# Kernel tuning notes

Hardware: AMD Instinct MI355X
Metric: run time of the kernel (lower is better)

The kernel has to match this reference:

```python
import jax, jax.numpy as jnp
import numpy as np

SEQ, BATCH, HID = 2048, 4, 1024


def setup_inputs() -> dict:
    key = jax.random.key(0)
    ks = jax.random.split(key, 8)
    s = 1.0 / np.sqrt(HID)
    return {
        "x": jax.random.normal(ks[0], (SEQ, BATCH, HID), dtype=jnp.float32),
        "ssm": jax.random.uniform(ks[1], (BATCH, SEQ, SEQ), dtype=jnp.float32),
        "Wq": jax.random.uniform(ks[2], (HID, HID), jnp.float32, -s, s),
        "bq": jax.random.uniform(ks[3], (HID,), jnp.float32, -s, s),
        "Wk": jax.random.uniform(ks[4], (HID, HID), jnp.float32, -s, s),
        "bk": jax.random.uniform(ks[5], (HID,), jnp.float32, -s, s),
        "Wv": jax.random.uniform(ks[6], (HID, HID), jnp.float32, -s, s),
        "bv": jax.random.uniform(ks[7], (HID,), jnp.float32, -s, s),
    }


def reference(x, ssm, Wq, bq, Wk, bk, Wv, bv):
    # x: [seq, batch, hid]; torch Linear: y = x @ W.T + b
    scale = jnp.asarray(HID ** 0.5, x.dtype)
    Q = x @ Wq.T + bq                      # [s, b, h]
    K = x @ Wk.T + bk
    V = x @ Wv.T + bv
    # transpose to batch-first: [b, s, h]
    Q = jnp.transpose(Q, (1, 0, 2))
    K = jnp.transpose(K, (1, 0, 2))
    V = jnp.transpose(V, (1, 0, 2))
    scores = jnp.einsum('bqh,bkh->bqk', Q, K) / scale   # [b, s, s]
    masked = scores * ssm                                # multiplicative mask on raw scores
    attn = jax.nn.softmax(masked, axis=-1)
    out = jnp.einsum('bqk,bkh->bqh', attn, V)            # [b, s, h]
    return jnp.transpose(out, (1, 0, 2))                 # [s, b, h]
```

## Files before the change

### kernel.cpp

```cpp
#include <hip/hip_runtime.h>
#include <hip/hip_bf16.h>

#define SEQ 2048
#define BATCH 4
#define HID 1024

typedef __bf16 bf16x8 __attribute__((ext_vector_type(8)));
typedef __bf16 bf16x4 __attribute__((ext_vector_type(4)));
typedef float f32x4 __attribute__((ext_vector_type(4)));

__device__ __forceinline__ void gload_lds16(void* lds, const void* g) {
  __builtin_amdgcn_global_load_lds(
      (const __attribute__((address_space(1))) void*)g,
      (__attribute__((address_space(3))) void*)lds, 16, 0, 0);
}

__global__ __launch_bounds__(256) void cast_f32_bf16(const float* __restrict__ in,
                                                     __bf16* __restrict__ out, int n8) {
  int i = blockIdx.x * 256 + threadIdx.x;
  if (i >= n8) return;
  const float4* p = (const float4*)in + (size_t)i * 2;
  float4 a = p[0], b = p[1];
  bf16x8 v;
  v[0] = (__bf16)a.x; v[1] = (__bf16)a.y; v[2] = (__bf16)a.z; v[3] = (__bf16)a.w;
  v[4] = (__bf16)b.x; v[5] = (__bf16)b.y; v[6] = (__bf16)b.z; v[7] = (__bf16)b.w;
  ((bf16x8*)out)[i] = v;
}

__global__ __launch_bounds__(256) void cast_w3(const float* __restrict__ w0,
                                               const float* __restrict__ w1,
                                               const float* __restrict__ w2,
                                               __bf16* __restrict__ out) {
  const int wsel = blockIdx.y;
  const float* src = wsel == 0 ? w0 : wsel == 1 ? w1 : w2;
  int i = blockIdx.x * 256 + threadIdx.x;
  const float4* p = (const float4*)src + (size_t)i * 2;
  float4 a = p[0], b = p[1];
  bf16x8 v;
  v[0] = (__bf16)a.x; v[1] = (__bf16)a.y; v[2] = (__bf16)a.z; v[3] = (__bf16)a.w;
  v[4] = (__bf16)b.x; v[5] = (__bf16)b.y; v[6] = (__bf16)b.z; v[7] = (__bf16)b.w;
  ((bf16x8*)(out + (size_t)wsel * HID * HID))[i] = v;
}

__global__ void concat_bias(const float* b0, const float* b1, const float* b2,
                            float* __restrict__ out) {
  const float* s = blockIdx.x == 0 ? b0 : blockIdx.x == 1 ? b1 : b2;
  out[blockIdx.x * HID + threadIdx.x] = s[threadIdx.x];
}

#define SLOT 49152
template<int EPI>
__global__ __launch_bounds__(512, 2)
void gemm8(const __bf16* __restrict__ A, int lda, long long sAz,
           const __bf16* __restrict__ B, int ldb, long long sBz,
           const float* __restrict__ aux, void* __restrict__ dst,
           float* __restrict__ aux2, int K)
{
  __shared__ __align__(16) char lds[3 * SLOT];
  const int tid = threadIdx.x;
  const int wid = tid >> 6, lane = tid & 63;
  const int wr = wid >> 2, wc = wid & 3;
  const int m0 = blockIdx.x * 128, n0 = blockIdx.y * 256;
  const int z = blockIdx.z;
  const __bf16* Ab = A + (size_t)z * sAz;
  const __bf16* Bb = B + (size_t)z * sBz;

  const int srow = tid >> 3;
  const int scol = ((tid & 7) * 16) ^ ((srow & 7) << 4);
  const char* asrc0 = (const char*)(Ab + (size_t)(m0 + srow) * lda) + scol;
  const char* asrc1 = (const char*)(Ab + (size_t)(m0 + srow + 64) * lda) + scol;
  const char* bsrc0 = (const char*)(Bb + (size_t)(n0 + srow) * ldb) + scol;
  const char* bsrc1 = (const char*)(Bb + (size_t)(n0 + srow + 64) * ldb) + scol;
  const char* bsrc2 = (const char*)(Bb + (size_t)(n0 + srow + 128) * ldb) + scol;
  const char* bsrc3 = (const char*)(Bb + (size_t)(n0 + srow + 192) * ldb) + scol;
  const int dA = tid * 16, dB = 16384 + tid * 16;

  const int fr = lane & 15, fq = lane >> 4;
  const int fc2 = fq * 16;
  const int swz = (fr & 7) << 4;
  int aoff[4][2], boff[4][2];
#pragma unroll
  for (int mi = 0; mi < 4; ++mi) {
    const int row = wr * 64 + mi * 16 + fr;
#pragma unroll
    for (int ks = 0; ks < 2; ++ks)
      aoff[mi][ks] = row * 128 + ((fc2 + ks * 64) ^ swz);
  }
#pragma unroll
  for (int ni = 0; ni < 4; ++ni) {
    const int row = wc * 64 + ni * 16 + fr;
#pragma unroll
    for (int ks = 0; ks < 2; ++ks)
      boff[ni][ks] = 16384 + row * 128 + ((fc2 + ks * 64) ^ swz);
  }

  const int nk = K >> 6;
  {
    char* s0 = lds;
    gload_lds16(s0 + dA, asrc0); gload_lds16(s0 + dA + 8192, asrc1);
    gload_lds16(s0 + dB, bsrc0); gload_lds16(s0 + dB + 8192, bsrc1);
    gload_lds16(s0 + dB + 16384, bsrc2); gload_lds16(s0 + dB + 24576, bsrc3);
    char* s1 = lds + SLOT;
    gload_lds16(s1 + dA, asrc0 + 128); gload_lds16(s1 + dA + 8192, asrc1 + 128);
    gload_lds16(s1 + dB, bsrc0 + 128); gload_lds16(s1 + dB + 8192, bsrc1 + 128);
    gload_lds16(s1 + dB + 16384, bsrc2 + 128); gload_lds16(s1 + dB + 24576, bsrc3 + 128);
  }

  f32x4 acc[4][4] = {};
  for (int t = 0; t < nk; ++t) {
    char* s = lds + (t % 3) * SLOT;
    if (t + 1 < nk) asm volatile("s_waitcnt vmcnt(6)" ::: "memory");
    else            asm volatile("s_waitcnt vmcnt(0)" ::: "memory");
    __builtin_amdgcn_s_barrier();
    asm volatile("" ::: "memory");

    bf16x8 a[4][2], b[4][2];
#pragma unroll
    for (int mi = 0; mi < 4; ++mi)
#pragma unroll
      for (int ks = 0; ks < 2; ++ks)
        a[mi][ks] = *(const bf16x8*)(s + aoff[mi][ks]);
#pragma unroll
    for (int ni = 0; ni < 2; ++ni)
#pragma unroll
      for (int ks = 0; ks < 2; ++ks)
        b[ni][ks] = *(const bf16x8*)(s + boff[ni][ks]);
    if (t + 2 < nk) {
      char* sn = lds + ((t + 2) % 3) * SLOT;
      const size_t ko = (size_t)(t + 2) * 128;
      gload_lds16(sn + dA, asrc0 + ko);
      gload_lds16(sn + dA + 8192, asrc1 + ko);
      gload_lds16(sn + dB, bsrc0 + ko);
    }
    asm volatile("" ::: "memory");
    __builtin_amdgcn_s_barrier();
    asm volatile("s_waitcnt lgkmcnt(0)" ::: "memory");
    __builtin_amdgcn_sched_barrier(0);
    __builtin_amdgcn_s_setprio(1);
#pragma unroll
    for (int mi = 0; mi < 4; ++mi)
#pragma unroll
      for (int ni = 0; ni < 2; ++ni)
#pragma unroll
        for (int ks = 0; ks < 2; ++ks)
          acc[mi][ni] = __builtin_amdgcn_mfma_f32_16x16x32_bf16(a[mi][ks], b[ni][ks], acc[mi][ni], 0, 0, 0);
    __builtin_amdgcn_s_setprio(0);
    asm volatile("" ::: "memory");
    __builtin_amdgcn_s_barrier();
    asm volatile("" ::: "memory");

#pragma unroll
    for (int ni = 2; ni < 4; ++ni)
#pragma unroll
      for (int ks = 0; ks < 2; ++ks)
        b[ni][ks] = *(const bf16x8*)(s + boff[ni][ks]);
    if (t + 2 < nk) {
      char* sn = lds + ((t + 2) % 3) * SLOT;
      const size_t ko = (size_t)(t + 2) * 128;
      gload_lds16(sn + dB + 8192, bsrc1 + ko);
      gload_lds16(sn + dB + 16384, bsrc2 + ko);
      gload_lds16(sn + dB + 24576, bsrc3 + ko);
    }
    asm volatile("" ::: "memory");
    __builtin_amdgcn_s_barrier();
    asm volatile("s_waitcnt lgkmcnt(0)" ::: "memory");
    __builtin_amdgcn_sched_barrier(0);
    __builtin_amdgcn_s_setprio(1);
#pragma unroll
    for (int mi = 0; mi < 4; ++mi)
#pragma unroll
      for (int ni = 2; ni < 4; ++ni)
#pragma unroll
        for (int ks = 0; ks < 2; ++ks)
          acc[mi][ni] = __builtin_amdgcn_mfma_f32_16x16x32_bf16(a[mi][ks], b[ni][ks], acc[mi][ni], 0, 0, 0);
    __builtin_amdgcn_s_setprio(0);
  }
  __syncthreads();

  if (EPI == 0) {
    const int hsel = n0 >> 10;
    const size_t BSH = (size_t)BATCH * SEQ * HID;
#pragma unroll
    for (int mi = 0; mi < 4; ++mi) {
#pragma unroll
      for (int ni = 0; ni < 4; ++ni) {
        const int gn = n0 + wc * 64 + ni * 16 + fr;
        const int h = gn & (HID - 1);
        const int gmb = m0 + wr * 64 + mi * 16 + fq * 4;
        const float bias = aux[gn];
        f32x4 v = acc[mi][ni];
        if (hsel < 2) {
#pragma unroll
          for (int r = 0; r < 4; ++r)
            ((__bf16*)dst)[(size_t)hsel * BSH + (size_t)z * SEQ * HID +
                           (size_t)(gmb + r) * HID + h] = (__bf16)(v[r] + bias);
        } else {
          bf16x4 vv;
#pragma unroll
          for (int r = 0; r < 4; ++r) vv[r] = (__bf16)(v[r] + bias);
          *(bf16x4*)&((__bf16*)dst)[2 * BSH + (size_t)z * HID * SEQ +
                                    (size_t)h * SEQ + gmb] = vv;
        }
      }
    }
  } else if (EPI == 2) {
    float psum[4][4] = {};
#pragma unroll
    for (int mi = 0; mi < 4; ++mi) {
#pragma unroll
      for (int ni = 0; ni < 4; ++ni) {
        const int gn = n0 + wc * 64 + ni * 16 + fr;
        const int gmb = m0 + wr * 64 + mi * 16 + fq * 4;
        f32x4 v = acc[mi][ni];
#pragma unroll
        for (int r = 0; r < 4; ++r) {
          const size_t idx = (size_t)z * SEQ * SEQ + (size_t)(gmb + r) * SEQ + gn;
          const float e = __expf(v[r] * 0.03125f * aux[idx]);
          ((__bf16*)dst)[idx] = (__bf16)e;
          psum[mi][r] += e;
        }
      }
    }
#pragma unroll
    for (int mi = 0; mi < 4; ++mi)
#pragma unroll
      for (int r = 0; r < 4; ++r) {
        float sv = psum[mi][r];
        sv += __shfl_xor(sv, 1); sv += __shfl_xor(sv, 2);
        sv += __shfl_xor(sv, 4); sv += __shfl_xor(sv, 8);
        psum[mi][r] = sv;
      }
    float* red = (float*)lds;
    if (fr == 0) {
#pragma unroll
      for (int mi = 0; mi < 4; ++mi)
#pragma unroll
        for (int r = 0; r < 4; ++r)
          red[wid * 64 + mi * 16 + fq * 4 + r] = psum[mi][r];
    }
    __syncthreads();
    if (tid < 128) {
      const int half = tid >> 6, r64 = tid & 63;
      float sv = 0.f;
#pragma unroll
      for (int j = 0; j < 4; ++j) sv += red[(half * 4 + j) * 64 + r64];
      aux2[((size_t)z * SEQ + m0 + tid) * 8 + blockIdx.y] = sv;
    }
  } else {
    float* red = (float*)lds;
    if (tid < 128) {
      const float* pp = aux + ((size_t)z * SEQ + m0 + tid) * 8;
      float sv = 0.f;
#pragma unroll
      for (int j = 0; j < 8; ++j) sv += pp[j];
      red[tid] = 1.f / sv;
    }
    __syncthreads();
#pragma unroll
    for (int mi = 0; mi < 4; ++mi) {
#pragma unroll
      for (int ni = 0; ni < 4; ++ni) {
        const int gn = n0 + wc * 64 + ni * 16 + fr;
        const int rbase = wr * 64 + mi * 16 + fq * 4;
        f32x4 v = acc[mi][ni];
#pragma unroll
        for (int r = 0; r < 4; ++r)
          ((float*)dst)[((size_t)(m0 + rbase + r) * BATCH + z) * HID + gn] = v[r] * red[rbase + r];
      }
    }
  }
}

extern "C" void kernel_launch(void* const* d_in, const int* in_sizes, int n_in,
                              void* d_out, int out_size, void* d_ws, size_t ws_size,
                              hipStream_t stream) {
  const float* x   = (const float*)d_in[0];
  const float* ssm = (const float*)d_in[1];
  const float* Wq  = (const float*)d_in[2];
  const float* bq  = (const float*)d_in[3];
  const float* Wk  = (const float*)d_in[4];
  const float* bk  = (const float*)d_in[5];
  const float* Wv  = (const float*)d_in[6];
  const float* bv  = (const float*)d_in[7];
  float* out = (float*)d_out;

  const size_t BSH = (size_t)BATCH * SEQ * HID;
  float* bqkv    = (float*)d_ws;
  float* partial = bqkv + 4096;
  __bf16* xbf  = (__bf16*)(partial + (size_t)BATCH * SEQ * 8);
  __bf16* wqkv = xbf + BSH;
  __bf16* Qb = wqkv + (size_t)3 * HID * HID;
  __bf16* Kb = Qb + BSH;
  __bf16* Vt = Qb + 2 * BSH;
  __bf16* E  = Qb + 3 * BSH;

  cast_f32_bf16<<<(int)(BSH / 8 / 256), 256, 0, stream>>>(x, xbf, (int)(BSH / 8));
  cast_w3<<<dim3(HID * HID / 8 / 256, 3), 256, 0, stream>>>(Wq, Wk, Wv, wqkv);
  concat_bias<<<3, HID, 0, stream>>>(bq, bk, bv, bqkv);

  gemm8<0><<<dim3(16, 12, BATCH), 512, 0, stream>>>(xbf, BATCH * HID, HID,
                                                    wqkv, HID, 0, bqkv, Qb, nullptr, HID);
  gemm8<2><<<dim3(16, 8, BATCH), 512, 0, stream>>>(Qb, HID, (long long)SEQ * HID,
                                                   Kb, HID, (long long)SEQ * HID,
                                                   ssm, E, partial, HID);
  gemm8<3><<<dim3(16, 4, BATCH), 512, 0, stream>>>(E, SEQ, (long long)SEQ * SEQ,
                                                   Vt, SEQ, (long long)HID * SEQ,
                                                   partial, out, nullptr, SEQ);
}
```

Baseline: 165.4 us.

## Enlarge GEMM tiles to 256 rows with double-buffered four-phase MFMA schedule

Replaces the 128x256 triple-buffered GEMM with a templated 256xNW*64 tile kernel that uses two LDS buffers and splits each K-step into four MFMA phases interleaved with staged loads. The QKV projection now treats x as a flat 8192-row matrix instead of batching over z, and the epilogue remaps rows to batch/seq. The PV GEMM uses a narrower 256x128 tile. The aim is more data reuse per LDS load and fewer blocks, at the cost of more accumulator registers (risking spills at 2 blocks/CU), double rather than triple buffering, and scalar V-transposed stores in the QKV epilogue.

```diff
diff --git a/kernel.cpp b/kernel.cpp
--- a/kernel.cpp
+++ b/kernel.cpp
@@ -6,7 +6,6 @@
 #define HID 1024
 
 typedef __bf16 bf16x8 __attribute__((ext_vector_type(8)));
-typedef __bf16 bf16x4 __attribute__((ext_vector_type(4)));
 typedef float f32x4 __attribute__((ext_vector_type(4)));
 
 __device__ __forceinline__ void gload_lds16(void* lds, const void* g) {
@@ -48,169 +47,190 @@
   out[blockIdx.x * HID + threadIdx.x] = s[threadIdx.x];
 }
 
-#define SLOT 49152
-template<int EPI>
+template<int EPI, int NW>
 __global__ __launch_bounds__(512, 2)
-void gemm8(const __bf16* __restrict__ A, int lda, long long sAz,
-           const __bf16* __restrict__ B, int ldb, long long sBz,
-           const float* __restrict__ aux, void* __restrict__ dst,
-           float* __restrict__ aux2, int K)
+void gemm256(const __bf16* __restrict__ A, int lda, long long sAz,
+             const __bf16* __restrict__ B, int ldb, long long sBz,
+             const float* __restrict__ aux, void* __restrict__ dst,
+             float* __restrict__ aux2, int K)
 {
-  __shared__ __align__(16) char lds[3 * SLOT];
+  constexpr int SLOTB = 32768 + NW * 8192;
+  __shared__ __align__(16) char lds[2 * SLOTB];
   const int tid = threadIdx.x;
   const int wid = tid >> 6, lane = tid & 63;
   const int wr = wid >> 2, wc = wid & 3;
-  const int m0 = blockIdx.x * 128, n0 = blockIdx.y * 256;
+  const int m0 = blockIdx.x * 256, n0 = blockIdx.y * (NW * 64);
   const int z = blockIdx.z;
   const __bf16* Ab = A + (size_t)z * sAz;
   const __bf16* Bb = B + (size_t)z * sBz;
 
   const int srow = tid >> 3;
-  const int scol = ((tid & 7) * 16) ^ ((srow & 7) << 4);
-  const char* asrc0 = (const char*)(Ab + (size_t)(m0 + srow) * lda) + scol;
-  const char* asrc1 = (const char*)(Ab + (size_t)(m0 + srow + 64) * lda) + scol;
-  const char* bsrc0 = (const char*)(Bb + (size_t)(n0 + srow) * ldb) + scol;
-  const char* bsrc1 = (const char*)(Bb + (size_t)(n0 + srow + 64) * ldb) + scol;
-  const char* bsrc2 = (const char*)(Bb + (size_t)(n0 + srow + 128) * ldb) + scol;
-  const char* bsrc3 = (const char*)(Bb + (size_t)(n0 + srow + 192) * ldb) + scol;
-  const int dA = tid * 16, dB = 16384 + tid * 16;
+  const int ssw = ((tid & 7) * 16) ^ ((srow & 7) << 4);
+  const char* ap0 = (const char*)(Ab + (size_t)(m0 + srow) * lda) + ssw;
+  const char* ap1 = (const char*)(Ab + (size_t)(m0 + 64 + srow) * lda) + ssw;
+  const char* ap2 = (const char*)(Ab + (size_t)(m0 + 128 + srow) * lda) + ssw;
+  const char* ap3 = (const char*)(Ab + (size_t)(m0 + 192 + srow) * lda) + ssw;
+  const char* bp0 = (const char*)(Bb + (size_t)(n0 + srow) * ldb) + ssw;
+  const char* bp1 = (const char*)(Bb + (size_t)(n0 + 64 + srow) * ldb) + ssw;
+  const char* bp2 = NW == 4 ? (const char*)(Bb + (size_t)(n0 + 128 + srow) * ldb) + ssw : nullptr;
+  const char* bp3 = NW == 4 ? (const char*)(Bb + (size_t)(n0 + 192 + srow) * ldb) + ssw : nullptr;
+  const int dA = tid * 16, dB = 32768 + tid * 16;
+
+  auto STAGE0 = [&](char* sb, size_t ko) {
+    gload_lds16(sb + dA, ap0 + ko);
+    gload_lds16(sb + dA + 8192, ap1 + ko);
+    gload_lds16(sb + dB, bp0 + ko);
+    if (NW == 4) gload_lds16(sb + dB + 8192, bp1 + ko);
+  };
+  auto STAGE1 = [&](char* sb, size_t ko) {
+    gload_lds16(sb + dA + 16384, ap2 + ko);
+    gload_lds16(sb + dA + 24576, ap3 + ko);
+    if (NW == 4) {
+      gload_lds16(sb + dB + 16384, bp2 + ko);
+      gload_lds16(sb + dB + 24576, bp3 + ko);
+    } else {
+      gload_lds16(sb + dB + 8192, bp1 + ko);
+    }
+  };
 
   const int fr = lane & 15, fq = lane >> 4;
-  const int fc2 = fq * 16;
   const int swz = (fr & 7) << 4;
-  int aoff[4][2], boff[4][2];
-#pragma unroll
-  for (int mi = 0; mi < 4; ++mi) {
-    const int row = wr * 64 + mi * 16 + fr;
-#pragma unroll
-    for (int ks = 0; ks < 2; ++ks)
-      aoff[mi][ks] = row * 128 + ((fc2 + ks * 64) ^ swz);
-  }
-#pragma unroll
-  for (int ni = 0; ni < 4; ++ni) {
-    const int row = wc * 64 + ni * 16 + fr;
-#pragma unroll
-    for (int ks = 0; ks < 2; ++ks)
-      boff[ni][ks] = 16384 + row * 128 + ((fc2 + ks * 64) ^ swz);
-  }
+  const int c0 = (fq * 16) ^ swz;
+  const int c1 = (fq * 16 + 64) ^ swz;
+  const int abase = wr * 16384 + fr * 128;
+  const int bbase = 32768 + wc * (NW * 2048) + fr * 128;
 
   const int nk = K >> 6;
-  {
-    char* s0 = lds;
-    gload_lds16(s0 + dA, asrc0); gload_lds16(s0 + dA + 8192, asrc1);
-    gload_lds16(s0 + dB, bsrc0); gload_lds16(s0 + dB + 8192, bsrc1);
-    gload_lds16(s0 + dB + 16384, bsrc2); gload_lds16(s0 + dB + 24576, bsrc3);
-    char* s1 = lds + SLOT;
-    gload_lds16(s1 + dA, asrc0 + 128); gload_lds16(s1 + dA + 8192, asrc1 + 128);
-    gload_lds16(s1 + dB, bsrc0 + 128); gload_lds16(s1 + dB + 8192, bsrc1 + 128);
-    gload_lds16(s1 + dB + 16384, bsrc2 + 128); gload_lds16(s1 + dB + 24576, bsrc3 + 128);
-  }
-
-  f32x4 acc[4][4] = {};
+  STAGE0(lds, 0);
+  STAGE1(lds, 0);
+
+  f32x4 acc[8][NW] = {};
   for (int t = 0; t < nk; ++t) {
-    char* s = lds + (t % 3) * SLOT;
-    if (t + 1 < nk) asm volatile("s_waitcnt vmcnt(6)" ::: "memory");
-    else            asm volatile("s_waitcnt vmcnt(0)" ::: "memory");
-    __builtin_amdgcn_s_barrier();
-    asm volatile("" ::: "memory");
-
-    bf16x8 a[4][2], b[4][2];
-#pragma unroll
-    for (int mi = 0; mi < 4; ++mi)
-#pragma unroll
-      for (int ks = 0; ks < 2; ++ks)
-        a[mi][ks] = *(const bf16x8*)(s + aoff[mi][ks]);
-#pragma unroll
-    for (int ni = 0; ni < 2; ++ni)
-#pragma unroll
-      for (int ks = 0; ks < 2; ++ks)
-        b[ni][ks] = *(const bf16x8*)(s + boff[ni][ks]);
-    if (t + 2 < nk) {
-      char* sn = lds + ((t + 2) % 3) * SLOT;
-      const size_t ko = (size_t)(t + 2) * 128;
-      gload_lds16(sn + dA, asrc0 + ko);
-      gload_lds16(sn + dA + 8192, asrc1 + ko);
-      gload_lds16(sn + dB, bsrc0 + ko);
-    }
-    asm volatile("" ::: "memory");
-    __builtin_amdgcn_s_barrier();
+    char* sb = lds + (t & 1) * SLOTB;
+    char* sn = lds + ((t + 1) & 1) * SLOTB;
+    const size_t ko = (size_t)(t + 1) * 128;
+
+    asm volatile("s_waitcnt vmcnt(0)" ::: "memory");
+    __builtin_amdgcn_s_barrier();
+    asm volatile("" ::: "memory");
+
+    bf16x8 a0[4][2], a1[4][2], bb[NW][2];
+#pragma unroll
+    for (int m = 0; m < 4; ++m) {
+      a0[m][0] = *(const bf16x8*)(sb + abase + m * 2048 + c0);
+      a0[m][1] = *(const bf16x8*)(sb + abase + m * 2048 + c1);
+    }
+#pragma unroll
+    for (int n = 0; n < NW / 2; ++n) {
+      bb[n][0] = *(const bf16x8*)(sb + bbase + n * 2048 + c0);
+      bb[n][1] = *(const bf16x8*)(sb + bbase + n * 2048 + c1);
+    }
+#pragma unroll
+    for (int n = NW / 2; n < NW; ++n) {
+      bb[n][0] = *(const bf16x8*)(sb + bbase + n * 2048 + c0);
+      bb[n][1] = *(const bf16x8*)(sb + bbase + n * 2048 + c1);
+    }
+    if (t + 1 < nk) STAGE0(sn, ko);
+    asm volatile("" ::: "memory");
+    __builtin_amdgcn_s_barrier();
+    if (NW == 4) asm volatile("s_waitcnt lgkmcnt(4)" ::: "memory");
+    else         asm volatile("s_waitcnt lgkmcnt(2)" ::: "memory");
+    __builtin_amdgcn_sched_barrier(0);
+    __builtin_amdgcn_s_setprio(1);
+#pragma unroll
+    for (int m = 0; m < 4; ++m)
+#pragma unroll
+      for (int n = 0; n < NW / 2; ++n) {
+        acc[m][n] = __builtin_amdgcn_mfma_f32_16x16x32_bf16(a0[m][0], bb[n][0], acc[m][n], 0, 0, 0);
+        acc[m][n] = __builtin_amdgcn_mfma_f32_16x16x32_bf16(a0[m][1], bb[n][1], acc[m][n], 0, 0, 0);
+      }
+    __builtin_amdgcn_s_setprio(0);
+    asm volatile("" ::: "memory");
+    __builtin_amdgcn_s_barrier();
+    asm volatile("" ::: "memory");
+
+#pragma unroll
+    for (int m = 0; m < 4; ++m) {
+      a1[m][0] = *(const bf16x8*)(sb + abase + 8192 + m * 2048 + c0);
+      a1[m][1] = *(const bf16x8*)(sb + abase + 8192 + m * 2048 + c1);
+    }
+    if (t + 1 < nk) STAGE1(sn, ko);
+    asm volatile("" ::: "memory");
+    __builtin_amdgcn_s_barrier();
+    asm volatile("s_waitcnt lgkmcnt(8)" ::: "memory");
+    __builtin_amdgcn_sched_barrier(0);
+    __builtin_amdgcn_s_setprio(1);
+#pragma unroll
+    for (int m = 0; m < 4; ++m)
+#pragma unroll
+      for (int n = NW / 2; n < NW; ++n) {
+        acc[m][n] = __builtin_amdgcn_mfma_f32_16x16x32_bf16(a0[m][0], bb[n][0], acc[m][n], 0, 0, 0);
+        acc[m][n] = __builtin_amdgcn_mfma_f32_16x16x32_bf16(a0[m][1], bb[n][1], acc[m][n], 0, 0, 0);
+      }
+    __builtin_amdgcn_s_setprio(0);
+    asm volatile("" ::: "memory");
+    __builtin_amdgcn_s_barrier();
+    asm volatile("" ::: "memory");
+
     asm volatile("s_waitcnt lgkmcnt(0)" ::: "memory");
     __builtin_amdgcn_sched_barrier(0);
     __builtin_amdgcn_s_setprio(1);
 #pragma unroll
-    for (int mi = 0; mi < 4; ++mi)
-#pragma unroll
-      for (int ni = 0; ni < 2; ++ni)
-#pragma unroll
-        for (int ks = 0; ks < 2; ++ks)
-          acc[mi][ni] = __builtin_amdgcn_mfma_f32_16x16x32_bf16(a[mi][ks], b[ni][ks], acc[mi][ni], 0, 0, 0);
+    for (int m = 0; m < 4; ++m)
+#pragma unroll
+      for (int n = NW / 2; n < NW; ++n) {
+        acc[4 + m][n] = __builtin_amdgcn_mfma_f32_16x16x32_bf16(a1[m][0], bb[n][0], acc[4 + m][n], 0, 0, 0);
+        acc[4 + m][n] = __builtin_amdgcn_mfma_f32_16x16x32_bf16(a1[m][1], bb[n][1], acc[4 + m][n], 0, 0, 0);
+      }
     __builtin_amdgcn_s_setprio(0);
     asm volatile("" ::: "memory");
     __builtin_amdgcn_s_barrier();
     asm volatile("" ::: "memory");
 
-#pragma unroll
-    for (int ni = 2; ni < 4; ++ni)
-#pragma unroll
-      for (int ks = 0; ks < 2; ++ks)
-        b[ni][ks] = *(const bf16x8*)(s + boff[ni][ks]);
-    if (t + 2 < nk) {
-      char* sn = lds + ((t + 2) % 3) * SLOT;
-      const size_t ko = (size_t)(t + 2) * 128;
-      gload_lds16(sn + dB + 8192, bsrc1 + ko);
-      gload_lds16(sn + dB + 16384, bsrc2 + ko);
-      gload_lds16(sn + dB + 24576, bsrc3 + ko);
-    }
-    asm volatile("" ::: "memory");
-    __builtin_amdgcn_s_barrier();
-    asm volatile("s_waitcnt lgkmcnt(0)" ::: "memory");
-    __builtin_amdgcn_sched_barrier(0);
     __builtin_amdgcn_s_setprio(1);
 #pragma unroll
-    for (int mi = 0; mi < 4; ++mi)
-#pragma unroll
-      for (int ni = 2; ni < 4; ++ni)
-#pragma unroll
-        for (int ks = 0; ks < 2; ++ks)
-          acc[mi][ni] = __builtin_amdgcn_mfma_f32_16x16x32_bf16(a[mi][ks], b[ni][ks], acc[mi][ni], 0, 0, 0);
+    for (int m = 0; m < 4; ++m)
+#pragma unroll
+      for (int n = 0; n < NW / 2; ++n) {
+        acc[4 + m][n] = __builtin_amdgcn_mfma_f32_16x16x32_bf16(a1[m][0], bb[n][0], acc[4 + m][n], 0, 0, 0);
+        acc[4 + m][n] = __builtin_amdgcn_mfma_f32_16x16x32_bf16(a1[m][1], bb[n][1], acc[4 + m][n], 0, 0, 0);
+      }
     __builtin_amdgcn_s_setprio(0);
   }
   __syncthreads();
 
   if (EPI == 0) {
-    const int hsel = n0 >> 10;
     const size_t BSH = (size_t)BATCH * SEQ * HID;
 #pragma unroll
-    for (int mi = 0; mi < 4; ++mi) {
-#pragma unroll
-      for (int ni = 0; ni < 4; ++ni) {
-        const int gn = n0 + wc * 64 + ni * 16 + fr;
-        const int h = gn & (HID - 1);
-        const int gmb = m0 + wr * 64 + mi * 16 + fq * 4;
+    for (int mi = 0; mi < 8; ++mi) {
+#pragma unroll
+      for (int ni = 0; ni < NW; ++ni) {
+        const int gn = n0 + wc * (NW * 16) + ni * 16 + fr;
+        const int hsel = gn >> 10, h = gn & (HID - 1);
+        const int gmb = m0 + wr * 128 + mi * 16 + fq * 4;
         const float bias = aux[gn];
         f32x4 v = acc[mi][ni];
-        if (hsel < 2) {
-#pragma unroll
-          for (int r = 0; r < 4; ++r)
-            ((__bf16*)dst)[(size_t)hsel * BSH + (size_t)z * SEQ * HID +
-                           (size_t)(gmb + r) * HID + h] = (__bf16)(v[r] + bias);
-        } else {
-          bf16x4 vv;
-#pragma unroll
-          for (int r = 0; r < 4; ++r) vv[r] = (__bf16)(v[r] + bias);
-          *(bf16x4*)&((__bf16*)dst)[2 * BSH + (size_t)z * HID * SEQ +
-                                    (size_t)h * SEQ + gmb] = vv;
+#pragma unroll
+        for (int r = 0; r < 4; ++r) {
+          const int gm = gmb + r;
+          const int b = gm & 3, s = gm >> 2;
+          if (hsel < 2)
+            ((__bf16*)dst)[(size_t)hsel * BSH + (size_t)b * SEQ * HID +
+                           (size_t)s * HID + h] = (__bf16)(v[r] + bias);
+          else
+            ((__bf16*)dst)[2 * BSH + (size_t)b * HID * SEQ +
+                           (size_t)h * SEQ + s] = (__bf16)(v[r] + bias);
         }
       }
     }
   } else if (EPI == 2) {
-    float psum[4][4] = {};
-#pragma unroll
-    for (int mi = 0; mi < 4; ++mi) {
-#pragma unroll
-      for (int ni = 0; ni < 4; ++ni) {
-        const int gn = n0 + wc * 64 + ni * 16 + fr;
-        const int gmb = m0 + wr * 64 + mi * 16 + fq * 4;
+    float psum[8][4] = {};
+#pragma unroll
+    for (int mi = 0; mi < 8; ++mi) {
+#pragma unroll
+      for (int ni = 0; ni < NW; ++ni) {
+        const int gn = n0 + wc * (NW * 16) + ni * 16 + fr;
+        const int gmb = m0 + wr * 128 + mi * 16 + fq * 4;
         f32x4 v = acc[mi][ni];
 #pragma unroll
         for (int r = 0; r < 4; ++r) {
@@ -222,7 +242,7 @@
       }
     }
 #pragma unroll
-    for (int mi = 0; mi < 4; ++mi)
+    for (int mi = 0; mi < 8; ++mi)
 #pragma unroll
       for (int r = 0; r < 4; ++r) {
         float sv = psum[mi][r];
@@ -233,22 +253,22 @@
     float* red = (float*)lds;
     if (fr == 0) {
 #pragma unroll
-      for (int mi = 0; mi < 4; ++mi)
+      for (int mi = 0; mi < 8; ++mi)
 #pragma unroll
         for (int r = 0; r < 4; ++r)
-          red[wid * 64 + mi * 16 + fq * 4 + r] = psum[mi][r];
+          red[wid * 128 + mi * 16 + fq * 4 + r] = psum[mi][r];
     }
     __syncthreads();
-    if (tid < 128) {
-      const int half = tid >> 6, r64 = tid & 63;
+    if (tid < 256) {
+      const int wrr = tid >> 7, lrow = tid & 127;
       float sv = 0.f;
 #pragma unroll
-      for (int j = 0; j < 4; ++j) sv += red[(half * 4 + j) * 64 + r64];
+      for (int w = 0; w < 4; ++w) sv += red[(wrr * 4 + w) * 128 + lrow];
       aux2[((size_t)z * SEQ + m0 + tid) * 8 + blockIdx.y] = sv;
     }
   } else {
     float* red = (float*)lds;
-    if (tid < 128) {
+    if (tid < 256) {
       const float* pp = aux + ((size_t)z * SEQ + m0 + tid) * 8;
       float sv = 0.f;
 #pragma unroll
@@ -257,11 +277,11 @@
     }
     __syncthreads();
 #pragma unroll
-    for (int mi = 0; mi < 4; ++mi) {
-#pragma unroll
-      for (int ni = 0; ni < 4; ++ni) {
-        const int gn = n0 + wc * 64 + ni * 16 + fr;
-        const int rbase = wr * 64 + mi * 16 + fq * 4;
+    for (int mi = 0; mi < 8; ++mi) {
+#pragma unroll
+      for (int ni = 0; ni < NW; ++ni) {
+        const int gn = n0 + wc * (NW * 16) + ni * 16 + fr;
+        const int rbase = wr * 128 + mi * 16 + fq * 4;
         f32x4 v = acc[mi][ni];
 #pragma unroll
         for (int r = 0; r < 4; ++r)
@@ -298,12 +318,12 @@
   cast_w3<<<dim3(HID * HID / 8 / 256, 3), 256, 0, stream>>>(Wq, Wk, Wv, wqkv);
   concat_bias<<<3, HID, 0, stream>>>(bq, bk, bv, bqkv);
 
-  gemm8<0><<<dim3(16, 12, BATCH), 512, 0, stream>>>(xbf, BATCH * HID, HID,
-                                                    wqkv, HID, 0, bqkv, Qb, nullptr, HID);
-  gemm8<2><<<dim3(16, 8, BATCH), 512, 0, stream>>>(Qb, HID, (long long)SEQ * HID,
+  gemm256<0, 4><<<dim3(32, 12, 1), 512, 0, stream>>>(xbf, HID, 0,
+                                                     wqkv, HID, 0, bqkv, Qb, nullptr, HID);
+  gemm256<2, 4><<<dim3(8, 8, 4), 512, 0, stream>>>(Qb, HID, (long long)SEQ * HID,
                                                    Kb, HID, (long long)SEQ * HID,
                                                    ssm, E, partial, HID);
-  gemm8<3><<<dim3(16, 4, BATCH), 512, 0, stream>>>(E, SEQ, (long long)SEQ * SEQ,
+  gemm256<3, 2><<<dim3(8, 8, 4), 512, 0, stream>>>(E, SEQ, (long long)SEQ * SEQ,
                                                    Vt, SEQ, (long long)HID * SEQ,
                                                    partial, out, nullptr, SEQ);
 }
```

Result: slower. 230.6 us (+39.4%).

## Add 256x256-tile double-buffered GEMM for QKV projection and score kernels

Applied to the files above, without the earlier changes.

Adds a new gemm3p kernel that computes 256x256 output tiles with a 64-wide K step, a two-slot LDS double buffer, XOR-swizzled LDS addressing and loads staged in three sub-phases that overlap the MFMA work. The QKV projection now treats x as one flat 8192x1024 matrix instead of four strided batches. The score/exp kernel also moves to the larger tile. The existing gemm8, still used for the final PV GEMM, is simplified to load all of B at once with fewer barriers per K step. The goal is more data reuse per tile and less barrier overhead, at the cost of higher register pressure from 128 accumulators and fewer blocks in the grid.

```diff
diff --git a/kernel.cpp b/kernel.cpp
--- a/kernel.cpp
+++ b/kernel.cpp
@@ -46,6 +46,214 @@
                             float* __restrict__ out) {
   const float* s = blockIdx.x == 0 ? b0 : blockIdx.x == 1 ? b1 : b2;
   out[blockIdx.x * HID + threadIdx.x] = s[threadIdx.x];
+}
+
+template<int EPI>
+__global__ __launch_bounds__(512, 2)
+void gemm3p(const __bf16* __restrict__ A, int lda, long long sAz,
+            const __bf16* __restrict__ B, int ldb, long long sBz,
+            const float* __restrict__ aux, void* __restrict__ dst,
+            float* __restrict__ aux2, int K)
+{
+  __shared__ __align__(16) char lds[2 * 65536];
+  const int tid = threadIdx.x;
+  const int wid = tid >> 6, lane = tid & 63;
+  const int wr = wid >> 2, wc = wid & 3;
+  const int m0 = blockIdx.x * 256, n0 = blockIdx.y * 256;
+  const int z = blockIdx.z;
+  const __bf16* Ab = A + (size_t)z * sAz;
+  const __bf16* Bb = B + (size_t)z * sBz;
+
+  const int srow = tid >> 3;
+  const int scol = ((tid & 7) * 16) ^ ((srow & 7) << 4);
+  const char* a0s = (const char*)(Ab + (size_t)(m0 + srow) * lda) + scol;
+  const char* a1s = (const char*)(Ab + (size_t)(m0 + 64 + srow) * lda) + scol;
+  const char* a2s = (const char*)(Ab + (size_t)(m0 + 128 + srow) * lda) + scol;
+  const char* a3s = (const char*)(Ab + (size_t)(m0 + 192 + srow) * lda) + scol;
+  const char* b0s = (const char*)(Bb + (size_t)(n0 + srow) * ldb) + scol;
+  const char* b1s = (const char*)(Bb + (size_t)(n0 + 64 + srow) * ldb) + scol;
+  const char* b2s = (const char*)(Bb + (size_t)(n0 + 128 + srow) * ldb) + scol;
+  const char* b3s = (const char*)(Bb + (size_t)(n0 + 192 + srow) * ldb) + scol;
+  const int dT = tid * 16;
+
+  auto U0 = [&](char* sb, size_t ko) {
+    gload_lds16(sb + dT, a0s + ko);
+    gload_lds16(sb + 8192 + dT, a1s + ko);
+    gload_lds16(sb + 32768 + dT, b0s + ko);
+    gload_lds16(sb + 40960 + dT, b1s + ko);
+  };
+  auto U1 = [&](char* sb, size_t ko) {
+    gload_lds16(sb + 49152 + dT, b2s + ko);
+    gload_lds16(sb + 57344 + dT, b3s + ko);
+  };
+  auto U2 = [&](char* sb, size_t ko) {
+    gload_lds16(sb + 16384 + dT, a2s + ko);
+    gload_lds16(sb + 24576 + dT, a3s + ko);
+  };
+
+  const int fr = lane & 15, fq = lane >> 4;
+  const int swz = (fr & 7) << 4;
+  const int c0 = (fq * 16) ^ swz;
+  const int arow = (wr * 64 + fr) * 128;
+  const int brow = 32768 + (wc * 32 + fr) * 128;
+
+  const int nk = K >> 6;
+  U0(lds, 0); U1(lds, 0); U2(lds, 0);
+
+  f32x4 acc[8][4] = {};
+  for (int t = 0; t < nk; ++t) {
+    char* sb = lds + (t & 1) * 65536;
+    char* sn = lds + ((t + 1) & 1) * 65536;
+    const size_t ko = (size_t)(t + 1) * 128;
+    const bool more = (t + 1 < nk);
+
+    bf16x8 a[4][2], b0[2][2], b1[2][2];
+    asm volatile("s_waitcnt vmcnt(4)" ::: "memory");
+    __builtin_amdgcn_s_barrier();
+    asm volatile("" ::: "memory");
+#pragma unroll
+    for (int mi = 0; mi < 4; ++mi)
+#pragma unroll
+      for (int ks = 0; ks < 2; ++ks)
+        a[mi][ks] = *(const bf16x8*)(sb + arow + mi * 2048 + (c0 ^ (ks << 6)));
+#pragma unroll
+    for (int ni = 0; ni < 2; ++ni)
+#pragma unroll
+      for (int ks = 0; ks < 2; ++ks)
+        b0[ni][ks] = *(const bf16x8*)(sb + brow + ni * 2048 + (c0 ^ (ks << 6)));
+    if (more) U0(sn, ko);
+    asm volatile("s_waitcnt lgkmcnt(0)" ::: "memory");
+    __builtin_amdgcn_sched_barrier(0);
+    __builtin_amdgcn_s_setprio(1);
+#pragma unroll
+    for (int mi = 0; mi < 4; ++mi)
+#pragma unroll
+      for (int ni = 0; ni < 2; ++ni)
+#pragma unroll
+        for (int ks = 0; ks < 2; ++ks)
+          acc[mi][ni] = __builtin_amdgcn_mfma_f32_16x16x32_bf16(a[mi][ks], b0[ni][ks], acc[mi][ni], 0, 0, 0);
+    __builtin_amdgcn_s_setprio(0);
+
+    if (more) asm volatile("s_waitcnt vmcnt(6)" ::: "memory");
+    else      asm volatile("s_waitcnt vmcnt(2)" ::: "memory");
+    __builtin_amdgcn_s_barrier();
+    asm volatile("" ::: "memory");
+#pragma unroll
+    for (int ni = 0; ni < 2; ++ni)
+#pragma unroll
+      for (int ks = 0; ks < 2; ++ks)
+        b1[ni][ks] = *(const bf16x8*)(sb + brow + 16384 + ni * 2048 + (c0 ^ (ks << 6)));
+    if (more) U1(sn, ko);
+    asm volatile("s_waitcnt lgkmcnt(0)" ::: "memory");
+    __builtin_amdgcn_sched_barrier(0);
+    __builtin_amdgcn_s_setprio(1);
+#pragma unroll
+    for (int mi = 0; mi < 4; ++mi)
+#pragma unroll
+      for (int ni = 0; ni < 2; ++ni)
+#pragma unroll
+        for (int ks = 0; ks < 2; ++ks)
+          acc[mi][2 + ni] = __builtin_amdgcn_mfma_f32_16x16x32_bf16(a[mi][ks], b1[ni][ks], acc[mi][2 + ni], 0, 0, 0);
+    __builtin_amdgcn_s_setprio(0);
+
+    if (more) asm volatile("s_waitcnt vmcnt(6)" ::: "memory");
+    else      asm volatile("s_waitcnt vmcnt(0)" ::: "memory");
+    __builtin_amdgcn_s_barrier();
+    asm volatile("" ::: "memory");
+#pragma unroll
+    for (int mi = 0; mi < 4; ++mi)
+#pragma unroll
+      for (int ks = 0; ks < 2; ++ks)
+        a[mi][ks] = *(const bf16x8*)(sb + arow + 16384 + mi * 2048 + (c0 ^ (ks << 6)));
+    if (more) U2(sn, ko);
+    asm volatile("s_waitcnt lgkmcnt(0)" ::: "memory");
+    __builtin_amdgcn_sched_barrier(0);
+    __builtin_amdgcn_s_setprio(1);
+#pragma unroll
+    for (int mi = 0; mi < 4; ++mi)
+#pragma unroll
+      for (int ks = 0; ks < 2; ++ks) {
+#pragma unroll
+        for (int ni = 0; ni < 2; ++ni)
+          acc[4 + mi][ni] = __builtin_amdgcn_mfma_f32_16x16x32_bf16(a[mi][ks], b0[ni][ks], acc[4 + mi][ni], 0, 0, 0);
+#pragma unroll
+        for (int ni = 0; ni < 2; ++ni)
+          acc[4 + mi][2 + ni] = __builtin_amdgcn_mfma_f32_16x16x32_bf16(a[mi][ks], b1[ni][ks], acc[4 + mi][2 + ni], 0, 0, 0);
+      }
+    __builtin_amdgcn_s_setprio(0);
+  }
+  asm volatile("s_waitcnt vmcnt(0)" ::: "memory");
+  __syncthreads();
+
+  if (EPI == 0) {
+    const size_t BSH = (size_t)BATCH * SEQ * HID;
+#pragma unroll
+    for (int mi = 0; mi < 8; ++mi) {
+      const int rbase = (mi < 4 ? wr * 64 + mi * 16 : 128 + wr * 64 + (mi - 4) * 16) + fq * 4;
+#pragma unroll
+      for (int ni = 0; ni < 4; ++ni) {
+        const int gn = n0 + (ni < 2 ? wc * 32 + ni * 16 : 128 + wc * 32 + (ni - 2) * 16) + fr;
+        const int hsel = gn >> 10, h = gn & (HID - 1);
+        const float bias = aux[gn];
+        f32x4 v = acc[mi][ni];
+#pragma unroll
+        for (int r = 0; r < 4; ++r) {
+          const int gm = m0 + rbase + r;
+          const int b = gm & 3, s = gm >> 2;
+          if (hsel < 2)
+            ((__bf16*)dst)[(size_t)hsel * BSH + (size_t)b * SEQ * HID +
+                           (size_t)s * HID + h] = (__bf16)(v[r] + bias);
+          else
+            ((__bf16*)dst)[2 * BSH + (size_t)b * HID * SEQ +
+                           (size_t)h * SEQ + s] = (__bf16)(v[r] + bias);
+        }
+      }
+    }
+  } else {
+    float psum[8][4] = {};
+#pragma unroll
+    for (int mi = 0; mi < 8; ++mi) {
+      const int rbase = (mi < 4 ? wr * 64 + mi * 16 : 128 + wr * 64 + (mi - 4) * 16) + fq * 4;
+#pragma unroll
+      for (int ni = 0; ni < 4; ++ni) {
+        const int gn = n0 + (ni < 2 ? wc * 32 + ni * 16 : 128 + wc * 32 + (ni - 2) * 16) + fr;
+        f32x4 v = acc[mi][ni];
+#pragma unroll
+        for (int r = 0; r < 4; ++r) {
+          const size_t idx = (size_t)z * SEQ * SEQ + (size_t)(m0 + rbase + r) * SEQ + gn;
+          const float e = __expf(v[r] * 0.03125f * aux[idx]);
+          ((__bf16*)dst)[idx] = (__bf16)e;
+          psum[mi][r] += e;
+        }
+      }
+    }
+#pragma unroll
+    for (int mi = 0; mi < 8; ++mi)
+#pragma unroll
+      for (int r = 0; r < 4; ++r) {
+        float sv = psum[mi][r];
+        sv += __shfl_xor(sv, 1); sv += __shfl_xor(sv, 2);
+        sv += __shfl_xor(sv, 4); sv += __shfl_xor(sv, 8);
+        psum[mi][r] = sv;
+      }
+    float* red = (float*)lds;
+    if (fr == 0) {
+#pragma unroll
+      for (int mi = 0; mi < 8; ++mi) {
+        const int rbase = (mi < 4 ? wr * 64 + mi * 16 : 128 + wr * 64 + (mi - 4) * 16) + fq * 4;
+#pragma unroll
+        for (int r = 0; r < 4; ++r)
+          red[wc * 256 + rbase + r] = psum[mi][r];
+      }
+    }
+    __syncthreads();
+    if (tid < 256) {
+      float sv = 0.f;
+#pragma unroll
+      for (int w = 0; w < 4; ++w) sv += red[w * 256 + tid];
+      aux2[((size_t)z * SEQ + m0 + tid) * 8 + blockIdx.y] = sv;
+    }
+  }
 }
 
 #define SLOT 49152
@@ -121,132 +329,35 @@
       for (int ks = 0; ks < 2; ++ks)
         a[mi][ks] = *(const bf16x8*)(s + aoff[mi][ks]);
 #pragma unroll
-    for (int ni = 0; ni < 2; ++ni)
+    for (int ni = 0; ni < 4; ++ni)
 #pragma unroll
       for (int ks = 0; ks < 2; ++ks)
         b[ni][ks] = *(const bf16x8*)(s + boff[ni][ks]);
+
     if (t + 2 < nk) {
       char* sn = lds + ((t + 2) % 3) * SLOT;
       const size_t ko = (size_t)(t + 2) * 128;
       gload_lds16(sn + dA, asrc0 + ko);
       gload_lds16(sn + dA + 8192, asrc1 + ko);
       gload_lds16(sn + dB, bsrc0 + ko);
-    }
-    asm volatile("" ::: "memory");
-    __builtin_amdgcn_s_barrier();
-    asm volatile("s_waitcnt lgkmcnt(0)" ::: "memory");
-    __builtin_amdgcn_sched_barrier(0);
+      gload_lds16(sn + dB + 8192, bsrc1 + ko);
+      gload_lds16(sn + dB + 16384, bsrc2 + ko);
+      gload_lds16(sn + dB + 24576, bsrc3 + ko);
+    }
+
     __builtin_amdgcn_s_setprio(1);
 #pragma unroll
     for (int mi = 0; mi < 4; ++mi)
 #pragma unroll
-      for (int ni = 0; ni < 2; ++ni)
+      for (int ni = 0; ni < 4; ++ni)
 #pragma unroll
         for (int ks = 0; ks < 2; ++ks)
           acc[mi][ni] = __builtin_amdgcn_mfma_f32_16x16x32_bf16(a[mi][ks], b[ni][ks], acc[mi][ni], 0, 0, 0);
     __builtin_amdgcn_s_setprio(0);
-    asm volatile("" ::: "memory");
-    __builtin_amdgcn_s_barrier();
-    asm volatile("" ::: "memory");
-
-#pragma unroll
-    for (int ni = 2; ni < 4; ++ni)
-#pragma unroll
-      for (int ks = 0; ks < 2; ++ks)
-        b[ni][ks] = *(const bf16x8*)(s + boff[ni][ks]);
-    if (t + 2 < nk) {
-      char* sn = lds + ((t + 2) % 3) * SLOT;
-      const size_t ko = (size_t)(t + 2) * 128;
-      gload_lds16(sn + dB + 8192, bsrc1 + ko);
-      gload_lds16(sn + dB + 16384, bsrc2 + ko);
-      gload_lds16(sn + dB + 24576, bsrc3 + ko);
-    }
-    asm volatile("" ::: "memory");
-    __builtin_amdgcn_s_barrier();
-    asm volatile("s_waitcnt lgkmcnt(0)" ::: "memory");
-    __builtin_amdgcn_sched_barrier(0);
-    __builtin_amdgcn_s_setprio(1);
-#pragma unroll
-    for (int mi = 0; mi < 4; ++mi)
-#pragma unroll
-      for (int ni = 2; ni < 4; ++ni)
-#pragma unroll
-        for (int ks = 0; ks < 2; ++ks)
-          acc[mi][ni] = __builtin_amdgcn_mfma_f32_16x16x32_bf16(a[mi][ks], b[ni][ks], acc[mi][ni], 0, 0, 0);
-    __builtin_amdgcn_s_setprio(0);
   }
   __syncthreads();
 
-  if (EPI == 0) {
-    const int hsel = n0 >> 10;
-    const size_t BSH = (size_t)BATCH * SEQ * HID;
-#pragma unroll
-    for (int mi = 0; mi < 4; ++mi) {
-#pragma unroll
-      for (int ni = 0; ni < 4; ++ni) {
-        const int gn = n0 + wc * 64 + ni * 16 + fr;
-        const int h = gn & (HID - 1);
-        const int gmb = m0 + wr * 64 + mi * 16 + fq * 4;
-        const float bias = aux[gn];
-        f32x4 v = acc[mi][ni];
-        if (hsel < 2) {
-#pragma unroll
-          for (int r = 0; r < 4; ++r)
-            ((__bf16*)dst)[(size_t)hsel * BSH + (size_t)z * SEQ * HID +
-                           (size_t)(gmb + r) * HID + h] = (__bf16)(v[r] + bias);
-        } else {
-          bf16x4 vv;
-#pragma unroll
-          for (int r = 0; r < 4; ++r) vv[r] = (__bf16)(v[r] + bias);
-          *(bf16x4*)&((__bf16*)dst)[2 * BSH + (size_t)z * HID * SEQ +
-                                    (size_t)h * SEQ + gmb] = vv;
-        }
-      }
-    }
-  } else if (EPI == 2) {
-    float psum[4][4] = {};
-#pragma unroll
-    for (int mi = 0; mi < 4; ++mi) {
-#pragma unroll
-      for (int ni = 0; ni < 4; ++ni) {
-        const int gn = n0 + wc * 64 + ni * 16 + fr;
-        const int gmb = m0 + wr * 64 + mi * 16 + fq * 4;
-        f32x4 v = acc[mi][ni];
-#pragma unroll
-        for (int r = 0; r < 4; ++r) {
-          const size_t idx = (size_t)z * SEQ * SEQ + (size_t)(gmb + r) * SEQ + gn;
-          const float e = __expf(v[r] * 0.03125f * aux[idx]);
-          ((__bf16*)dst)[idx] = (__bf16)e;
-          psum[mi][r] += e;
-        }
-      }
-    }
-#pragma unroll
-    for (int mi = 0; mi < 4; ++mi)
-#pragma unroll
-      for (int r = 0; r < 4; ++r) {
-        float sv = psum[mi][r];
-        sv += __shfl_xor(sv, 1); sv += __shfl_xor(sv, 2);
-        sv += __shfl_xor(sv, 4); sv += __shfl_xor(sv, 8);
-        psum[mi][r] = sv;
-      }
-    float* red = (float*)lds;
-    if (fr == 0) {
-#pragma unroll
-      for (int mi = 0; mi < 4; ++mi)
-#pragma unroll
-        for (int r = 0; r < 4; ++r)
-          red[wid * 64 + mi * 16 + fq * 4 + r] = psum[mi][r];
-    }
-    __syncthreads();
-    if (tid < 128) {
-      const int half = tid >> 6, r64 = tid & 63;
-      float sv = 0.f;
-#pragma unroll
-      for (int j = 0; j < 4; ++j) sv += red[(half * 4 + j) * 64 + r64];
-      aux2[((size_t)z * SEQ + m0 + tid) * 8 + blockIdx.y] = sv;
-    }
-  } else {
+  if (EPI == 3) {
     float* red = (float*)lds;
     if (tid < 128) {
       const float* pp = aux + ((size_t)z * SEQ + m0 + tid) * 8;
@@ -298,12 +409,12 @@
   cast_w3<<<dim3(HID * HID / 8 / 256, 3), 256, 0, stream>>>(Wq, Wk, Wv, wqkv);
   concat_bias<<<3, HID, 0, stream>>>(bq, bk, bv, bqkv);
 
-  gemm8<0><<<dim3(16, 12, BATCH), 512, 0, stream>>>(xbf, BATCH * HID, HID,
-                                                    wqkv, HID, 0, bqkv, Qb, nullptr, HID);
-  gemm8<2><<<dim3(16, 8, BATCH), 512, 0, stream>>>(Qb, HID, (long long)SEQ * HID,
-                                                   Kb, HID, (long long)SEQ * HID,
-                                                   ssm, E, partial, HID);
-  gemm8<3><<<dim3(16, 4, BATCH), 512, 0, stream>>>(E, SEQ, (long long)SEQ * SEQ,
-                                                   Vt, SEQ, (long long)HID * SEQ,
-                                                   partial, out, nullptr, SEQ);
-}
+  gemm3p<0><<<dim3(32, 12, 1), 512, 0, stream>>>(xbf, HID, 0,
+                                                 wqkv, HID, 0, bqkv, Qb, nullptr, HID);
+  gemm3p<2><<<dim3(8, 8, 4), 512, 0, stream>>>(Qb, HID, (long long)SEQ * HID,
+                                               Kb, HID, (long long)SEQ * HID,
+                                               ssm, E, partial, HID);
+  gemm8<3><<<dim3(16, 4, 4), 512, 0, stream>>>(E, SEQ, (long long)SEQ * SEQ,
+                                               Vt, SEQ, (long long)HID * SEQ,
+                                               partial, out, nullptr, SEQ);
+}
```

After: 185.7 us. 1.12x slower.
